# Kernel tuning notes

Hardware: AMD Instinct MI355X
Metric: run time of the kernel (lower is better)

## Reference

```python
import jax, jax.numpy as jnp
import numpy as np

B, N, CS, CZ, H, C, PQ, PV = 1, 512, 384, 128, 12, 16, 4, 8
INF, EPS = 1e5, 1e-8


def _quat_to_rot(q):
    # q: [..., 4] unit quaternion -> [..., 3, 3] rotation matrix
    w, x, y, z = q[..., 0], q[..., 1], q[..., 2], q[..., 3]
    r0 = jnp.stack([1 - 2 * (y * y + z * z), 2 * (x * y - w * z), 2 * (x * z + w * y)], -1)
    r1 = jnp.stack([2 * (x * y + w * z), 1 - 2 * (x * x + z * z), 2 * (y * z - w * x)], -1)
    r2 = jnp.stack([2 * (x * z - w * y), 2 * (y * z + w * x), 1 - 2 * (x * x + y * y)], -1)
    return jnp.stack([r0, r1, r2], -2)


def setup_inputs() -> dict:
    key = jax.random.key(0)
    ks = jax.random.split(key, 20)
    sc = 0.02
    quat = jax.random.normal(ks[0], (B, N, 4), jnp.float32)
    quat = quat / jnp.linalg.norm(quat, axis=-1, keepdims=True)
    concat_dim = H * (C + PV * 4 + CZ)
    return {
        "s": jax.random.normal(ks[1], (B, N, CS), jnp.float32),
        "z": jax.random.normal(ks[2], (B, N, N, CZ), jnp.float32),
        "rot": _quat_to_rot(quat),
        "trans": jax.random.normal(ks[3], (B, N, 3), jnp.float32),
        "mask": jnp.ones((B, N), jnp.float32),
        "W_q": jax.random.normal(ks[4], (CS, H * C), jnp.float32) * sc,
        "b_q": jnp.zeros((H * C,), jnp.float32),
        "W_kv": jax.random.normal(ks[5], (CS, 2 * H * C), jnp.float32) * sc,
        "b_kv": jnp.zeros((2 * H * C,), jnp.float32),
        "W_qp": jax.random.normal(ks[6], (CS, H * PQ * 3), jnp.float32) * sc,
        "b_qp": jnp.zeros((H * PQ * 3,), jnp.float32),
        "W_kvp": jax.random.normal(ks[7], (CS, H * (PQ + PV) * 3), jnp.float32) * sc,
        "b_kvp": jnp.zeros((H * (PQ + PV) * 3,), jnp.float32),
        "W_b": jax.random.normal(ks[8], (CZ, H), jnp.float32) * sc,
        "b_b": jnp.zeros((H,), jnp.float32),
        "head_weights": jnp.full((H,), 0.541324854612918, jnp.float32),  # softplus^-1(1)
        "W_out": jax.random.normal(ks[9], (concat_dim, CS), jnp.float32) * sc,
        "b_out": jnp.zeros((CS,), jnp.float32),
    }


def reference(s, z, rot, trans, mask, W_q, b_q, W_kv, b_kv, W_qp, b_qp, W_kvp, b_kvp,
              W_b, b_b, head_weights, W_out, b_out):
    # scalar projections
    q = (s @ W_q + b_q).reshape(*s.shape[:-1], H, C)              # [B,N,H,C]
    kv = (s @ W_kv + b_kv).reshape(*s.shape[:-1], H, 2 * C)
    k, v = kv[..., :C], kv[..., C:]                               # [B,N,H,C]

    def to_global_pts(lin, npts):
        # lin: [B,N,H*npts*3]; torch layout: split into thirds -> stack as xyz
        p = jnp.stack(jnp.split(lin, 3, axis=-1), axis=-1)        # [B,N,H*npts,3]
        g = jnp.einsum('bnij,bnpj->bnpi', rot, p) + trans[:, :, None, :]
        return g.reshape(*g.shape[:-2], H, npts, 3)

    q_pts = to_global_pts(s @ W_qp + b_qp, PQ)                    # [B,N,H,PQ,3]
    kv_pts = to_global_pts(s @ W_kvp + b_kvp, PQ + PV)
    k_pts, v_pts = kv_pts[..., :PQ, :], kv_pts[..., PQ:, :]       # [B,N,H,PQ/PV,3]

    # attention logits
    bias = z @ W_b + b_b                                          # [B,N,N,H]
    a = jnp.einsum('bihc,bjhc->bhij', q, k) * np.sqrt(1.0 / (3 * C))
    a = a + np.sqrt(1.0 / 3.0) * jnp.transpose(bias, (0, 3, 1, 2))

    d = q_pts[:, :, None] - k_pts[:, None]                        # [B,N,N,H,PQ,3]
    pt_att = jnp.sum(d * d, axis=-1)                              # [B,N,N,H,PQ]
    hw = jax.nn.softplus(head_weights) * np.sqrt(1.0 / (3 * (PQ * 9.0 / 2)))
    pt_att = jnp.sum(pt_att * hw[None, None, None, :, None], axis=-1) * (-0.5)  # [B,N,N,H]
    a = a + jnp.transpose(pt_att, (0, 3, 1, 2))

    sq_mask = INF * (mask[:, :, None] * mask[:, None, :] - 1.0)   # [B,N,N]
    a = jax.nn.softmax(a + sq_mask[:, None], axis=-1)             # [B,H,N,N]

    # aggregation
    o = jnp.einsum('bhij,bjhc->bihc', a, v).reshape(*s.shape[:-1], H * C)
    o_pt = jnp.einsum('bhij,bjhpc->bihpc', a, v_pts)              # [B,N,H,PV,3]
    o_pt = jnp.einsum('bnji,bnhpj->bnhpi', rot, o_pt - trans[:, :, None, None, :])
    o_pt_norm = jnp.sqrt(jnp.sum(o_pt ** 2, -1) + EPS).reshape(*s.shape[:-1], H * PV)
    o_pt = o_pt.reshape(*s.shape[:-1], H * PV, 3)
    o_pair = jnp.einsum('bhij,bijc->bihc', a, z).reshape(*s.shape[:-1], H * CZ)

    cat = jnp.concatenate([o, o_pt[..., 0], o_pt[..., 1], o_pt[..., 2], o_pt_norm, o_pair], -1)
    return cat @ W_out + b_out                                    # [B,N,CS]
```

## Files before the change

### kernel.cpp

```cpp
#include <hip/hip_runtime.h>
#include <hip/hip_bf16.h>
#include <math.h>


#define N_    512
#define CS_   384
#define INF_  100000.0f
#define EPS_  1e-8f

#define SC_QK 0.14433756729740643f
#define SC_B  0.5773502691896258f
#define SC_HW 0.13608276348795434f

__device__ __forceinline__ float softplus_(float x) {
    return (x > 20.f) ? x : log1pf(__expf(x));
}

__global__ __launch_bounds__(256) void proj_gemm(
    const float* __restrict__ A,
    const float* __restrict__ W0, const float* __restrict__ b0, float* __restrict__ C0, int N0,
    const float* __restrict__ W1, const float* __restrict__ b1, float* __restrict__ C1, int N1,
    const float* __restrict__ W2, const float* __restrict__ b2, float* __restrict__ C2, int N2,
    const float* __restrict__ W3, const float* __restrict__ b3, float* __restrict__ C3, int N3)
{
    const float* W; const float* bias; float* C; int Nt;
    switch (blockIdx.z) {
        case 0:  W = W0; bias = b0; C = C0; Nt = N0; break;
        case 1:  W = W1; bias = b1; C = C1; Nt = N1; break;
        case 2:  W = W2; bias = b2; C = C2; Nt = N2; break;
        default: W = W3; bias = b3; C = C3; Nt = N3; break;
    }
    const int n0 = blockIdx.y * 64;
    if (n0 >= Nt) return;
    const int m0 = blockIdx.x * 64;

    __shared__ float As[16 * 68];
    __shared__ float Bs[16 * 68];
    const int t  = threadIdx.x;
    const int tm = t & 15;
    const int tn = t >> 4;

    float acc[4][4];
    #pragma unroll
    for (int r = 0; r < 4; ++r)
        #pragma unroll
        for (int c = 0; c < 4; ++c) acc[r][c] = 0.f;

    for (int k0 = 0; k0 < CS_; k0 += 16) {
        {
            int m = t >> 2, kb = (t & 3) * 4;
            float4 a4 = *(const float4*)(A + (size_t)(m0 + m) * CS_ + k0 + kb);
            As[(kb + 0) * 68 + m] = a4.x;
            As[(kb + 1) * 68 + m] = a4.y;
            As[(kb + 2) * 68 + m] = a4.z;
            As[(kb + 3) * 68 + m] = a4.w;
        }
        {
            int kk = t >> 4, n = (t & 15) * 4;
            int gn = n0 + n;
            const float* wr = W + (size_t)(k0 + kk) * Nt;
            float4 b4;
            b4.x = (gn + 0 < Nt) ? wr[gn + 0] : 0.f;
            b4.y = (gn + 1 < Nt) ? wr[gn + 1] : 0.f;
            b4.z = (gn + 2 < Nt) ? wr[gn + 2] : 0.f;
            b4.w = (gn + 3 < Nt) ? wr[gn + 3] : 0.f;
            *(float4*)(Bs + kk * 68 + n) = b4;
        }
        __syncthreads();
        #pragma unroll
        for (int kk = 0; kk < 16; ++kk) {
            float4 a4 = *(const float4*)(As + kk * 68 + tm * 4);
            float4 b4 = *(const float4*)(Bs + kk * 68 + tn * 4);
            float am[4] = {a4.x, a4.y, a4.z, a4.w};
            float bn[4] = {b4.x, b4.y, b4.z, b4.w};
            #pragma unroll
            for (int r = 0; r < 4; ++r)
                #pragma unroll
                for (int c = 0; c < 4; ++c)
                    acc[r][c] = fmaf(am[r], bn[c], acc[r][c]);
        }
        __syncthreads();
    }
    #pragma unroll
    for (int r = 0; r < 4; ++r) {
        int gm = m0 + tm * 4 + r;
        int gn = n0 + tn * 4;
        float* cr = C + (size_t)gm * Nt;
        #pragma unroll
        for (int c = 0; c < 4; ++c)
            if (gn + c < Nt) cr[gn + c] = acc[r][c] + bias[gn + c];
    }
}

__global__ __launch_bounds__(192) void prep_points(
    const float* __restrict__ lqp, const float* __restrict__ lkvp,
    const float* __restrict__ rot, const float* __restrict__ trans,
    const float* __restrict__ kvb, const float* __restrict__ q,
    const float* __restrict__ hwraw,
    float* __restrict__ qp, float* __restrict__ kp,
    float* __restrict__ vcat, float* __restrict__ qcat,
    float* __restrict__ kcat, float* __restrict__ qn, float* __restrict__ kn)
{
    const int n = blockIdx.x;
    const int t = threadIdx.x;
    const float* R = rot   + n * 9;
    const float* T = trans + n * 3;

    if (t < 48) {
        float p0 = lqp[n * 144 + t];
        float p1 = lqp[n * 144 + 48 + t];
        float p2 = lqp[n * 144 + 96 + t];
        float* d = qp + n * 144 + t * 3;
        d[0] = R[0]*p0 + R[1]*p1 + R[2]*p2 + T[0];
        d[1] = R[3]*p0 + R[4]*p1 + R[5]*p2 + T[1];
        d[2] = R[6]*p0 + R[7]*p1 + R[8]*p2 + T[2];
    } else {
        int jj = t - 48;
        float p0 = lkvp[n * 432 + jj];
        float p1 = lkvp[n * 432 + 144 + jj];
        float p2 = lkvp[n * 432 + 288 + jj];
        float g0 = R[0]*p0 + R[1]*p1 + R[2]*p2 + T[0];
        float g1 = R[3]*p0 + R[4]*p1 + R[5]*p2 + T[1];
        float g2 = R[6]*p0 + R[7]*p1 + R[8]*p2 + T[2];
        int h = jj / 12, idx = jj % 12;
        if (idx < 4) {
            float* d = kp + n * 144 + (h * 4 + idx) * 3;
            d[0] = g0; d[1] = g1; d[2] = g2;
        } else {
            float* d = vcat + (size_t)n * 512 + 192 + h * 24 + (idx - 4) * 3;
            d[0] = g0; d[1] = g1; d[2] = g2;
        }
    }
    vcat[(size_t)n * 512 + t] = kvb[(size_t)n * 384 + (t >> 4) * 32 + 16 + (t & 15)];
    __syncthreads();

    {
        int h = t >> 4, c = t & 15;
        qcat[((size_t)h * 512 + n) * 28 + c] = q[(size_t)n * 192 + t];
        kcat[((size_t)h * 512 + n) * 28 + c] = kvb[(size_t)n * 384 + h * 32 + c] * SC_QK;
    }
    if (t < 144) {
        int h = t / 12;
        float hw = softplus_(hwraw[h]) * SC_HW;
        qcat[((size_t)h * 512 + n) * 28 + 16 + (t - h * 12)] = qp[n * 144 + t];
        kcat[((size_t)h * 512 + n) * 28 + 16 + (t - h * 12)] = kp[n * 144 + t] * hw;
    }
    if (t < 24) {
        int h = t % 12;
        float hw = softplus_(hwraw[h]) * SC_HW;
        const float* src = (t < 12) ? (qp + n * 144 + h * 12) : (kp + n * 144 + h * 12);
        float s = 0.f;
        #pragma unroll
        for (int r = 0; r < 12; ++r) { float v = src[r]; s = fmaf(v, v, s); }
        float* dst = (t < 12) ? qn : kn;
        dst[h * 512 + n] = 0.5f * hw * s;
    }
}

__global__ __launch_bounds__(256) void qkpt_gemm(
    const float* __restrict__ qcat, const float* __restrict__ kcat,
    const float* __restrict__ qn,   const float* __restrict__ kn,
    const float* __restrict__ mask, float* __restrict__ att)
{
    const int jt = blockIdx.x, it = blockIdx.y, h = blockIdx.z;
    __shared__ float As[28 * 68];
    __shared__ float Bs[28 * 68];
    __shared__ float qn_s[64], kn_s[64], mI[64], mJ[64];

    const int t  = threadIdx.x;
    const int tm = t & 15;
    const int tn = t >> 4;

    const float* Aq = qcat + ((size_t)h * 512 + it * 64) * 28;
    const float* Bk = kcat + ((size_t)h * 512 + jt * 64) * 28;
    for (int idx = t; idx < 448; idx += 256) {
        int row = idx / 7, c4 = idx % 7;
        float4 a4 = *(const float4*)(Aq + row * 28 + c4 * 4);
        As[(c4 * 4 + 0) * 68 + row] = a4.x;
        As[(c4 * 4 + 1) * 68 + row] = a4.y;
        As[(c4 * 4 + 2) * 68 + row] = a4.z;
        As[(c4 * 4 + 3) * 68 + row] = a4.w;
        float4 b4 = *(const float4*)(Bk + row * 28 + c4 * 4);
        Bs[(c4 * 4 + 0) * 68 + row] = b4.x;
        Bs[(c4 * 4 + 1) * 68 + row] = b4.y;
        Bs[(c4 * 4 + 2) * 68 + row] = b4.z;
        Bs[(c4 * 4 + 3) * 68 + row] = b4.w;
    }
    if (t < 64) {
        qn_s[t] = qn[h * 512 + it * 64 + t];
        mI[t]   = mask[it * 64 + t];
    } else if (t < 128) {
        kn_s[t - 64] = kn[h * 512 + jt * 64 + (t - 64)];
        mJ[t - 64]   = mask[jt * 64 + (t - 64)];
    }
    __syncthreads();

    float acc[4][4];
    #pragma unroll
    for (int r = 0; r < 4; ++r)
        #pragma unroll
        for (int c = 0; c < 4; ++c) acc[r][c] = 0.f;

    #pragma unroll
    for (int kk = 0; kk < 28; ++kk) {
        float4 a4 = *(const float4*)(As + kk * 68 + tm * 4);
        float4 b4 = *(const float4*)(Bs + kk * 68 + tn * 4);
        float am[4] = {a4.x, a4.y, a4.z, a4.w};
        float bn[4] = {b4.x, b4.y, b4.z, b4.w};
        #pragma unroll
        for (int r = 0; r < 4; ++r)
            #pragma unroll
            for (int c = 0; c < 4; ++c)
                acc[r][c] = fmaf(am[r], bn[c], acc[r][c]);
    }

    #pragma unroll
    for (int r = 0; r < 4; ++r) {
        const int i_ = it * 64 + tm * 4 + r;
        float* dst = att + ((size_t)h * 512 + i_) * 512 + jt * 64 + tn * 4;
        float4 o;
        float qnr = qn_s[tm * 4 + r], mir = mI[tm * 4 + r];
        o.x = acc[r][0] - qnr - kn_s[tn*4+0] + INF_ * (mir * mJ[tn*4+0] - 1.f);
        o.y = acc[r][1] - qnr - kn_s[tn*4+1] + INF_ * (mir * mJ[tn*4+1] - 1.f);
        o.z = acc[r][2] - qnr - kn_s[tn*4+2] + INF_ * (mir * mJ[tn*4+2] - 1.f);
        o.w = acc[r][3] - qnr - kn_s[tn*4+3] + INF_ * (mir * mJ[tn*4+3] - 1.f);
        *(float4*)dst = o;
    }
}

__global__ __launch_bounds__(256) void logits_k(
    const float* __restrict__ z, const float* __restrict__ Wb,
    const float* __restrict__ bb, float* __restrict__ att)
{
    __shared__ float ztile[64 * 132];
    const int jt   = blockIdx.x;
    const int i    = blockIdx.y;
    const int jb   = jt * 64;
    const int t    = threadIdx.x;
    const int lane = t & 63;

    const int h0 = __builtin_amdgcn_readfirstlane((t >> 6) * 3);
    const float bbA = bb[h0], bbB = bb[h0 + 1], bbC = bb[h0 + 2];

    const float4* zsrc = (const float4*)z + ((size_t)i * N_ + jb) * 32;
    #pragma unroll
    for (int k2 = 0; k2 < 8; ++k2) {
        int idx = t + k2 * 256;
        int rr = idx >> 5, c4 = idx & 31;
        *(float4*)(ztile + rr * 132 + c4 * 4) = zsrc[(size_t)rr * 32 + c4];
    }
    __syncthreads();

    float b0 = bbA, b1 = bbB, b2 = bbC;
    const float4* zrow = (const float4*)(ztile + lane * 132);
    #pragma unroll 8
    for (int c4 = 0; c4 < 32; ++c4) {
        float4 z4 = zrow[c4];
        float zc[4] = {z4.x, z4.y, z4.z, z4.w};
        #pragma unroll
        for (int cc = 0; cc < 4; ++cc) {
            const int c = c4 * 4 + cc;
            b0 = fmaf(zc[cc], Wb[c * 12 + h0    ], b0);
            b1 = fmaf(zc[cc], Wb[c * 12 + h0 + 1], b1);
            b2 = fmaf(zc[cc], Wb[c * 12 + h0 + 2], b2);
        }
    }

    const size_t base = ((size_t)h0 * 512 + i) * 512 + jb + lane;
    att[base]              = fmaf(SC_B, b0, att[base]);
    att[base + 262144]     = fmaf(SC_B, b1, att[base + 262144]);
    att[base + 2 * 262144] = fmaf(SC_B, b2, att[base + 2 * 262144]);
}

__global__ __launch_bounds__(384) void smax_av(
    float* __restrict__ att, const float* __restrict__ vcat,
    const float* __restrict__ rot, const float* __restrict__ trans,
    float* __restrict__ cat)
{
    __shared__ float a_s[12 * 516];
    __shared__ float opt_s[288];
    const int i    = blockIdx.x;
    const int t    = threadIdx.x;
    const int lane = t & 63;

    for (int idx = t; idx < 1536; idx += 384) {
        int h = idx >> 7, j4 = idx & 127;
        *(float4*)(a_s + h * 516 + j4 * 4) =
            *((const float4*)att + ((size_t)h * 512 + i) * 128 + j4);
    }
    __syncthreads();

    {
        const int w = t >> 6;
        #pragma unroll
        for (int hh = 0; hh < 2; ++hh) {
            const int h = w * 2 + hh;
            float* row = a_s + h * 516;
            float4 v0 = *(float4*)(row + lane * 8);
            float4 v1 = *(float4*)(row + lane * 8 + 4);
            float m = fmaxf(fmaxf(fmaxf(v0.x, v0.y), fmaxf(v0.z, v0.w)),
                            fmaxf(fmaxf(v1.x, v1.y), fmaxf(v1.z, v1.w)));
            #pragma unroll
            for (int off = 32; off > 0; off >>= 1)
                m = fmaxf(m, __shfl_xor(m, off));
            v0.x = __expf(v0.x - m); v0.y = __expf(v0.y - m);
            v0.z = __expf(v0.z - m); v0.w = __expf(v0.w - m);
            v1.x = __expf(v1.x - m); v1.y = __expf(v1.y - m);
            v1.z = __expf(v1.z - m); v1.w = __expf(v1.w - m);
            float s = v0.x + v0.y + v0.z + v0.w + v1.x + v1.y + v1.z + v1.w;
            #pragma unroll
            for (int off = 32; off > 0; off >>= 1)
                s += __shfl_xor(s, off);
            float inv = 1.f / s;
            v0.x *= inv; v0.y *= inv; v0.z *= inv; v0.w *= inv;
            v1.x *= inv; v1.y *= inv; v1.z *= inv; v1.w *= inv;
            *(float4*)(row + lane * 8)     = v0;
            *(float4*)(row + lane * 8 + 4) = v1;
        }
    }
    __syncthreads();

    for (int idx = t; idx < 1536; idx += 384) {
        int h = idx >> 7, j4 = idx & 127;
        *((float4*)att + ((size_t)h * 512 + i) * 128 + j4) =
            *(const float4*)(a_s + h * 516 + j4 * 4);
    }

    if (t < 240) {
        const int o0 = 2 * t;
        const int h  = (o0 < 192) ? (o0 >> 4) : ((o0 - 192) / 24);
        const float2* vrow = (const float2*)vcat + t;
        float accx = 0.f, accy = 0.f;
        #pragma unroll 8
        for (int j = 0; j < 512; ++j) {
            float2 v2 = vrow[(size_t)j * 256];
            float aj  = a_s[h * 516 + j];
            accx = fmaf(aj, v2.x, accx);
            accy = fmaf(aj, v2.y, accy);
        }
        if (o0 < 192) {
            cat[(size_t)i * 2112 + o0]     = accx;
            cat[(size_t)i * 2112 + o0 + 1] = accy;
        } else {
            opt_s[o0 - 192] = accx;
            opt_s[o0 - 191] = accy;
        }
    }
    __syncthreads();

    if (t < 96) {
        const float* R = rot   + i * 9;
        const float* T = trans + i * 3;
        float g0 = opt_s[t * 3 + 0] - T[0];
        float g1 = opt_s[t * 3 + 1] - T[1];
        float g2 = opt_s[t * 3 + 2] - T[2];
        float x  = R[0]*g0 + R[3]*g1 + R[6]*g2;
        float y  = R[1]*g0 + R[4]*g1 + R[7]*g2;
        float zz = R[2]*g0 + R[5]*g1 + R[8]*g2;
        float nrm = sqrtf(x*x + y*y + zz*zz + EPS_);
        float* cr = cat + (size_t)i * 2112;
        cr[192 + t] = x;
        cr[288 + t] = y;
        cr[384 + t] = zz;
        cr[480 + t] = nrm;
    }
}

__global__ __launch_bounds__(512) void opair_k(
    const float* __restrict__ att, const float* __restrict__ z,
    float* __restrict__ cat)
{
    __shared__ float pb[16 * 6 * 132];
    const int i  = blockIdx.x;
    const int t  = threadIdx.x;
    const int c4 = t & 31;
    const int jg = t >> 5;

    float4 acc[12];
    #pragma unroll
    for (int h = 0; h < 12; ++h) acc[h] = make_float4(0.f, 0.f, 0.f, 0.f);

    const float4* zr = (const float4*)z + (size_t)i * (N_ * 32) + c4;
    #pragma unroll 2
    for (int j4b = 0; j4b < 8; ++j4b) {
        const int jb = jg * 32 + j4b * 4;
        float4 zv[4];
        #pragma unroll
        for (int u = 0; u < 4; ++u) zv[u] = zr[(size_t)(jb + u) * 32];
        #pragma unroll
        for (int h = 0; h < 12; ++h) {
            float4 a4 = *(const float4*)(att + ((size_t)h * 512 + i) * 512 + jb);
            acc[h].x = fmaf(a4.x, zv[0].x, acc[h].x);
            acc[h].y = fmaf(a4.x, zv[0].y, acc[h].y);
            acc[h].z = fmaf(a4.x, zv[0].z, acc[h].z);
            acc[h].w = fmaf(a4.x, zv[0].w, acc[h].w);
            acc[h].x = fmaf(a4.y, zv[1].x, acc[h].x);
            acc[h].y = fmaf(a4.y, zv[1].y, acc[h].y);
            acc[h].z = fmaf(a4.y, zv[1].z, acc[h].z);
            acc[h].w = fmaf(a4.y, zv[1].w, acc[h].w);
            acc[h].x = fmaf(a4.z, zv[2].x, acc[h].x);
            acc[h].y = fmaf(a4.z, zv[2].y, acc[h].y);
            acc[h].z = fmaf(a4.z, zv[2].z, acc[h].z);
            acc[h].w = fmaf(a4.z, zv[2].w, acc[h].w);
            acc[h].x = fmaf(a4.w, zv[3].x, acc[h].x);
            acc[h].y = fmaf(a4.w, zv[3].y, acc[h].y);
            acc[h].z = fmaf(a4.w, zv[3].z, acc[h].z);
            acc[h].w = fmaf(a4.w, zv[3].w, acc[h].w);
        }
    }

    #pragma unroll
    for (int half = 0; half < 2; ++half) {
        __syncthreads();
        #pragma unroll
        for (int hh = 0; hh < 6; ++hh)
            *(float4*)(pb + (size_t)(jg * 6 + hh) * 132 + c4 * 4) = acc[half * 6 + hh];
        __syncthreads();
        #pragma unroll
        for (int k = 0; k < 2; ++k) {
            const int idx = t + k * 512;
            if (idx < 768) {
                const int hh = idx >> 7, c = idx & 127;
                float s = 0.f;
                #pragma unroll
                for (int g = 0; g < 16; ++g)
                    s += pb[(size_t)(g * 6 + hh) * 132 + c];
                cat[(size_t)i * 2112 + 576 + half * 768 + idx] = s;
            }
        }
    }
}

__global__ __launch_bounds__(256) void gemm_ksplit(
    const float* __restrict__ A, const float* __restrict__ W,
    float* __restrict__ P)
{
    const int kc = blockIdx.z;
    const int m0 = blockIdx.x * 64;
    const int n0 = blockIdx.y * 64;

    __shared__ float As[16 * 68];
    __shared__ float Bs[16 * 68];
    const int t  = threadIdx.x;
    const int tm = t & 15;
    const int tn = t >> 4;

    float acc[4][4];
    #pragma unroll
    for (int r = 0; r < 4; ++r)
        #pragma unroll
        for (int c = 0; c < 4; ++c) acc[r][c] = 0.f;

    const int kbeg = kc * 192;
    for (int k0 = kbeg; k0 < kbeg + 192; k0 += 16) {
        {
            int m = t >> 2, kb = (t & 3) * 4;
            float4 a4 = *(const float4*)(A + (size_t)(m0 + m) * 2112 + k0 + kb);
            As[(kb + 0) * 68 + m] = a4.x;
            As[(kb + 1) * 68 + m] = a4.y;
            As[(kb + 2) * 68 + m] = a4.z;
            As[(kb + 3) * 68 + m] = a4.w;
        }
        {
            int kk = t >> 4, n = (t & 15) * 4;
            float4 b4 = *(const float4*)(W + (size_t)(k0 + kk) * 384 + n0 + n);
            *(float4*)(Bs + kk * 68 + n) = b4;
        }
        __syncthreads();
        #pragma unroll
        for (int kk = 0; kk < 16; ++kk) {
            float4 a4 = *(const float4*)(As + kk * 68 + tm * 4);
            float4 b4 = *(const float4*)(Bs + kk * 68 + tn * 4);
            float am[4] = {a4.x, a4.y, a4.z, a4.w};
            float bn[4] = {b4.x, b4.y, b4.z, b4.w};
            #pragma unroll
            for (int r = 0; r < 4; ++r)
                #pragma unroll
                for (int c = 0; c < 4; ++c)
                    acc[r][c] = fmaf(am[r], bn[c], acc[r][c]);
        }
        __syncthreads();
    }
    float* Pk = P + (size_t)kc * (512 * 384);
    #pragma unroll
    for (int r = 0; r < 4; ++r) {
        int gm = m0 + tm * 4 + r;
        *(float4*)(Pk + (size_t)gm * 384 + n0 + tn * 4) =
            make_float4(acc[r][0], acc[r][1], acc[r][2], acc[r][3]);
    }
}

__global__ __launch_bounds__(256) void reduce_out(
    const float* __restrict__ P, const float* __restrict__ bias,
    float* __restrict__ out)
{
    int idx = blockIdx.x * 256 + threadIdx.x;
    const float4* b4 = (const float4*)bias;
    float4 s = b4[idx % 96];
    const float4* P4 = (const float4*)P;
    #pragma unroll
    for (int g = 0; g < 11; ++g) {
        float4 v = P4[(size_t)g * 49152 + idx];
        s.x += v.x; s.y += v.y; s.z += v.z; s.w += v.w;
    }
    ((float4*)out)[idx] = s;
}

extern "C" void kernel_launch(void* const* d_in, const int* in_sizes, int n_in,
                              void* d_out, int out_size, void* d_ws, size_t ws_size,
                              hipStream_t stream)
{
    const float* s     = (const float*)d_in[0];
    const float* z     = (const float*)d_in[1];
    const float* rot   = (const float*)d_in[2];
    const float* trans = (const float*)d_in[3];
    const float* mask  = (const float*)d_in[4];
    const float* W_q   = (const float*)d_in[5];
    const float* b_q   = (const float*)d_in[6];
    const float* W_kv  = (const float*)d_in[7];
    const float* b_kv  = (const float*)d_in[8];
    const float* W_qp  = (const float*)d_in[9];
    const float* b_qp  = (const float*)d_in[10];
    const float* W_kvp = (const float*)d_in[11];
    const float* b_kvp = (const float*)d_in[12];
    const float* W_b   = (const float*)d_in[13];
    const float* b_b   = (const float*)d_in[14];
    const float* hw    = (const float*)d_in[15];
    const float* W_out = (const float*)d_in[16];
    const float* b_out = (const float*)d_in[17];
    float* out = (float*)d_out;
    float* ws  = (float*)d_ws;

    float* att   = ws;
    float* cat   = att   + 3145728;
    float* q     = cat   + 1081344;
    float* kvb   = q     + 98304;
    float* lqp   = kvb   + 196608;
    float* lkvp  = lqp   + 73728;
    float* qp    = lkvp  + 221184;
    float* kp    = qp    + 73728;
    float* vcat  = kp    + 73728;
    float* qcat  = vcat  + 262144;
    float* kcat  = qcat  + 172032;
    float* qn    = kcat  + 172032;
    float* kn    = qn    + 6144;
    float* gpart = kn    + 6144;

    proj_gemm<<<dim3(8, 7, 4), 256, 0, stream>>>(
        s,
        W_q,   b_q,   q,    192,
        W_kv,  b_kv,  kvb,  384,
        W_qp,  b_qp,  lqp,  144,
        W_kvp, b_kvp, lkvp, 432);
    prep_points<<<512, 192, 0, stream>>>(lqp, lkvp, rot, trans, kvb, q, hw,
                                         qp, kp, vcat, qcat, kcat, qn, kn);
    qkpt_gemm<<<dim3(8, 8, 12), 256, 0, stream>>>(qcat, kcat, qn, kn, mask, att);
    logits_k<<<dim3(8, 512), 256, 0, stream>>>(z, W_b, b_b, att);
    smax_av<<<512, 384, 0, stream>>>(att, vcat, rot, trans, cat);
    opair_k<<<512, 512, 0, stream>>>(att, z, cat);
    gemm_ksplit<<<dim3(8, 6, 11), 256, 0, stream>>>(cat, W_out, gpart);
    reduce_out<<<192, 256, 0, stream>>>(gpart, b_out, out);
}
```

Baseline: 374.2 us.

## Fuse softmax, value aggregation and pair aggregation into one kernel

Merges the softmax/value-aggregation kernel and the pair-aggregation kernel into a single 512-thread kernel that keeps the normalized attention rows in shared memory. This drops the write-back of the softmaxed attention to global memory, the re-read of it by the pair kernel, and one kernel launch. The value aggregation is also restructured to split the j range over 4 thread groups with float4 loads and a shared-memory reduction. Shared memory is reused across phases, which adds synchronisation and raises the per-block footprint, and that may limit occupancy.

```diff
diff --git a/kernel.cpp b/kernel.cpp
--- a/kernel.cpp
+++ b/kernel.cpp
@@ -272,18 +272,22 @@
     att[base + 2 * 262144] = fmaf(SC_B, b2, att[base + 2 * 262144]);
 }
 
-__global__ __launch_bounds__(384) void smax_av(
-    float* __restrict__ att, const float* __restrict__ vcat,
-    const float* __restrict__ rot, const float* __restrict__ trans,
-    float* __restrict__ cat)
-{
-    __shared__ float a_s[12 * 516];
-    __shared__ float opt_s[288];
+__global__ __launch_bounds__(512) void attn_apply(
+    const float* __restrict__ att, const float* __restrict__ z,
+    const float* __restrict__ vcat, const float* __restrict__ rot,
+    const float* __restrict__ trans, float* __restrict__ cat)
+{
+    __shared__ float buf[12672];
+    float* a_s   = buf;
+    float* opt_s = buf + 6192;
+    float* pb_o  = buf + 6480;
+    float* pb    = buf;
+
     const int i    = blockIdx.x;
     const int t    = threadIdx.x;
     const int lane = t & 63;
 
-    for (int idx = t; idx < 1536; idx += 384) {
+    for (int idx = t; idx < 1536; idx += 512) {
         int h = idx >> 7, j4 = idx & 127;
         *(float4*)(a_s + h * 516 + j4 * 4) =
             *((const float4*)att + ((size_t)h * 512 + i) * 128 + j4);
@@ -294,7 +298,8 @@
         const int w = t >> 6;
         #pragma unroll
         for (int hh = 0; hh < 2; ++hh) {
-            const int h = w * 2 + hh;
+            if (hh == 1 && w >= 4) break;
+            const int h = (hh == 0) ? w : 8 + w;
             float* row = a_s + h * 516;
             float4 v0 = *(float4*)(row + lane * 8);
             float4 v1 = *(float4*)(row + lane * 8 + 4);
@@ -320,31 +325,46 @@
     }
     __syncthreads();
 
-    for (int idx = t; idx < 1536; idx += 384) {
-        int h = idx >> 7, j4 = idx & 127;
-        *((float4*)att + ((size_t)h * 512 + i) * 128 + j4) =
-            *(const float4*)(a_s + h * 516 + j4 * 4);
-    }
-
-    if (t < 240) {
-        const int o0 = 2 * t;
-        const int h  = (o0 < 192) ? (o0 >> 4) : ((o0 - 192) / 24);
-        const float2* vrow = (const float2*)vcat + t;
-        float accx = 0.f, accy = 0.f;
-        #pragma unroll 8
-        for (int j = 0; j < 512; ++j) {
-            float2 v2 = vrow[(size_t)j * 256];
-            float aj  = a_s[h * 516 + j];
-            accx = fmaf(aj, v2.x, accx);
-            accy = fmaf(aj, v2.y, accy);
-        }
-        if (o0 < 192) {
-            cat[(size_t)i * 2112 + o0]     = accx;
-            cat[(size_t)i * 2112 + o0 + 1] = accy;
-        } else {
-            opt_s[o0 - 192] = accx;
-            opt_s[o0 - 191] = accy;
-        }
+    {
+        const int jg = t & 3;
+        const int cq = t >> 2;
+        if (cq < 120) {
+            const int col = cq * 4;
+            const int h = (col < 192) ? (col >> 4) : ((col - 192) / 24);
+            const float* arow = a_s + h * 516;
+            const float4* vbase = (const float4*)vcat + cq;
+            float4 acc = make_float4(0.f, 0.f, 0.f, 0.f);
+            for (int jb = jg * 128; jb < jg * 128 + 128; jb += 4) {
+                float4 a4 = *(const float4*)(arow + jb);
+                float4 v0 = vbase[(size_t)(jb + 0) * 128];
+                float4 v1 = vbase[(size_t)(jb + 1) * 128];
+                float4 v2 = vbase[(size_t)(jb + 2) * 128];
+                float4 v3 = vbase[(size_t)(jb + 3) * 128];
+                acc.x = fmaf(a4.x, v0.x, acc.x);
+                acc.y = fmaf(a4.x, v0.y, acc.y);
+                acc.z = fmaf(a4.x, v0.z, acc.z);
+                acc.w = fmaf(a4.x, v0.w, acc.w);
+                acc.x = fmaf(a4.y, v1.x, acc.x);
+                acc.y = fmaf(a4.y, v1.y, acc.y);
+                acc.z = fmaf(a4.y, v1.z, acc.z);
+                acc.w = fmaf(a4.y, v1.w, acc.w);
+                acc.x = fmaf(a4.z, v2.x, acc.x);
+                acc.y = fmaf(a4.z, v2.y, acc.y);
+                acc.z = fmaf(a4.z, v2.z, acc.z);
+                acc.w = fmaf(a4.z, v2.w, acc.w);
+                acc.x = fmaf(a4.w, v3.x, acc.x);
+                acc.y = fmaf(a4.w, v3.y, acc.y);
+                acc.z = fmaf(a4.w, v3.z, acc.z);
+                acc.w = fmaf(a4.w, v3.w, acc.w);
+            }
+            *(float4*)(pb_o + jg * 484 + col) = acc;
+        }
+    }
+    __syncthreads();
+    if (t < 480) {
+        float s = pb_o[t] + pb_o[484 + t] + pb_o[968 + t] + pb_o[1452 + t];
+        if (t < 192) cat[(size_t)i * 2112 + t] = s;
+        else         opt_s[t - 192] = s;
     }
     __syncthreads();
 
@@ -364,68 +384,61 @@
         cr[384 + t] = zz;
         cr[480 + t] = nrm;
     }
-}
-
-__global__ __launch_bounds__(512) void opair_k(
-    const float* __restrict__ att, const float* __restrict__ z,
-    float* __restrict__ cat)
-{
-    __shared__ float pb[16 * 6 * 132];
-    const int i  = blockIdx.x;
-    const int t  = threadIdx.x;
-    const int c4 = t & 31;
-    const int jg = t >> 5;
-
-    float4 acc[12];
-    #pragma unroll
-    for (int h = 0; h < 12; ++h) acc[h] = make_float4(0.f, 0.f, 0.f, 0.f);
-
-    const float4* zr = (const float4*)z + (size_t)i * (N_ * 32) + c4;
-    #pragma unroll 2
-    for (int j4b = 0; j4b < 8; ++j4b) {
-        const int jb = jg * 32 + j4b * 4;
-        float4 zv[4];
-        #pragma unroll
-        for (int u = 0; u < 4; ++u) zv[u] = zr[(size_t)(jb + u) * 32];
-        #pragma unroll
-        for (int h = 0; h < 12; ++h) {
-            float4 a4 = *(const float4*)(att + ((size_t)h * 512 + i) * 512 + jb);
-            acc[h].x = fmaf(a4.x, zv[0].x, acc[h].x);
-            acc[h].y = fmaf(a4.x, zv[0].y, acc[h].y);
-            acc[h].z = fmaf(a4.x, zv[0].z, acc[h].z);
-            acc[h].w = fmaf(a4.x, zv[0].w, acc[h].w);
-            acc[h].x = fmaf(a4.y, zv[1].x, acc[h].x);
-            acc[h].y = fmaf(a4.y, zv[1].y, acc[h].y);
-            acc[h].z = fmaf(a4.y, zv[1].z, acc[h].z);
-            acc[h].w = fmaf(a4.y, zv[1].w, acc[h].w);
-            acc[h].x = fmaf(a4.z, zv[2].x, acc[h].x);
-            acc[h].y = fmaf(a4.z, zv[2].y, acc[h].y);
-            acc[h].z = fmaf(a4.z, zv[2].z, acc[h].z);
-            acc[h].w = fmaf(a4.z, zv[2].w, acc[h].w);
-            acc[h].x = fmaf(a4.w, zv[3].x, acc[h].x);
-            acc[h].y = fmaf(a4.w, zv[3].y, acc[h].y);
-            acc[h].z = fmaf(a4.w, zv[3].z, acc[h].z);
-            acc[h].w = fmaf(a4.w, zv[3].w, acc[h].w);
-        }
-    }
-
-    #pragma unroll
-    for (int half = 0; half < 2; ++half) {
-        __syncthreads();
-        #pragma unroll
-        for (int hh = 0; hh < 6; ++hh)
-            *(float4*)(pb + (size_t)(jg * 6 + hh) * 132 + c4 * 4) = acc[half * 6 + hh];
-        __syncthreads();
-        #pragma unroll
-        for (int k = 0; k < 2; ++k) {
-            const int idx = t + k * 512;
-            if (idx < 768) {
-                const int hh = idx >> 7, c = idx & 127;
-                float s = 0.f;
-                #pragma unroll
-                for (int g = 0; g < 16; ++g)
-                    s += pb[(size_t)(g * 6 + hh) * 132 + c];
-                cat[(size_t)i * 2112 + 576 + half * 768 + idx] = s;
+
+    {
+        const int c4 = t & 31;
+        const int jg = t >> 5;
+        float4 acc[12];
+        #pragma unroll
+        for (int h = 0; h < 12; ++h) acc[h] = make_float4(0.f, 0.f, 0.f, 0.f);
+
+        const float4* zr = (const float4*)z + (size_t)i * (N_ * 32) + c4;
+        #pragma unroll 2
+        for (int j4b = 0; j4b < 8; ++j4b) {
+            const int jb = jg * 32 + j4b * 4;
+            float4 zv[4];
+            #pragma unroll
+            for (int u = 0; u < 4; ++u) zv[u] = zr[(size_t)(jb + u) * 32];
+            #pragma unroll
+            for (int h = 0; h < 12; ++h) {
+                float4 a4 = *(const float4*)(a_s + h * 516 + jb);
+                acc[h].x = fmaf(a4.x, zv[0].x, acc[h].x);
+                acc[h].y = fmaf(a4.x, zv[0].y, acc[h].y);
+                acc[h].z = fmaf(a4.x, zv[0].z, acc[h].z);
+                acc[h].w = fmaf(a4.x, zv[0].w, acc[h].w);
+                acc[h].x = fmaf(a4.y, zv[1].x, acc[h].x);
+                acc[h].y = fmaf(a4.y, zv[1].y, acc[h].y);
+                acc[h].z = fmaf(a4.y, zv[1].z, acc[h].z);
+                acc[h].w = fmaf(a4.y, zv[1].w, acc[h].w);
+                acc[h].x = fmaf(a4.z, zv[2].x, acc[h].x);
+                acc[h].y = fmaf(a4.z, zv[2].y, acc[h].y);
+                acc[h].z = fmaf(a4.z, zv[2].z, acc[h].z);
+                acc[h].w = fmaf(a4.z, zv[2].w, acc[h].w);
+                acc[h].x = fmaf(a4.w, zv[3].x, acc[h].x);
+                acc[h].y = fmaf(a4.w, zv[3].y, acc[h].y);
+                acc[h].z = fmaf(a4.w, zv[3].z, acc[h].z);
+                acc[h].w = fmaf(a4.w, zv[3].w, acc[h].w);
+            }
+        }
+
+        #pragma unroll
+        for (int half = 0; half < 2; ++half) {
+            __syncthreads();
+            #pragma unroll
+            for (int hh = 0; hh < 6; ++hh)
+                *(float4*)(pb + (size_t)(jg * 6 + hh) * 132 + c4 * 4) = acc[half * 6 + hh];
+            __syncthreads();
+            #pragma unroll
+            for (int k = 0; k < 2; ++k) {
+                const int idx = t + k * 512;
+                if (idx < 768) {
+                    const int hh = idx >> 7, c = idx & 127;
+                    float s = 0.f;
+                    #pragma unroll
+                    for (int g = 0; g < 16; ++g)
+                        s += pb[(size_t)(g * 6 + hh) * 132 + c];
+                    cat[(size_t)i * 2112 + 576 + half * 768 + idx] = s;
+                }
             }
         }
     }
@@ -556,8 +569,7 @@
                                          qp, kp, vcat, qcat, kcat, qn, kn);
     qkpt_gemm<<<dim3(8, 8, 12), 256, 0, stream>>>(qcat, kcat, qn, kn, mask, att);
     logits_k<<<dim3(8, 512), 256, 0, stream>>>(z, W_b, b_b, att);
-    smax_av<<<512, 384, 0, stream>>>(att, vcat, rot, trans, cat);
-    opair_k<<<512, 512, 0, stream>>>(att, z, cat);
+    attn_apply<<<512, 512, 0, stream>>>(att, z, vcat, rot, trans, cat);
     gemm_ksplit<<<dim3(8, 6, 11), 256, 0, stream>>>(cat, W_out, gpart);
     reduce_out<<<192, 256, 0, stream>>>(gpart, b_out, out);
 }
```

Result: slower. 383.6 us (+2.5%).
